# Optimization experiments

Measured on AMD Instinct MI355X. Metric: run time of the kernel, lower is better.

Reference implementation:

```python
import jax, jax.numpy as jnp
import numpy as np

N_NODES = 10000
N_EDGES = 80000
IN_DIM = 512
H1, H2, OUT_DIM = 4096, 1024, 7
NEG_SLOPE = 0.2


def _gat_layer(x, src, dst, W, a_src, a_dst, b, n_nodes):
    # x: [N, F_in] -> h: [N, F_out]
    h = x @ W
    # per-edge attention logits: a_src . h_i + a_dst . h_j (PyG GATConv, heads=1)
    e = jax.nn.leaky_relu((h @ a_src)[src] + (h @ a_dst)[dst], NEG_SLOPE)
    # segment softmax over destination nodes
    m = jax.ops.segment_max(e, dst, num_segments=n_nodes)
    ex = jnp.exp(e - m[dst])
    denom = jax.ops.segment_sum(ex, dst, num_segments=n_nodes)
    alpha = ex / denom[dst]
    # scatter-add weighted messages
    out = jax.ops.segment_sum(alpha[:, None] * h[src], dst, num_segments=n_nodes)
    return out + b


def setup_inputs() -> dict:
    key = jax.random.key(0)
    ks = jax.random.split(key, 16)
    s = 0.05
    inp = {
        "x": jax.random.normal(ks[0], (N_NODES, IN_DIM), dtype=jnp.float32),
        "edge_index": jax.random.randint(ks[1], (2, N_EDGES), 0, N_NODES, dtype=jnp.int32),
        "W1": jax.random.normal(ks[2], (IN_DIM, H1), dtype=jnp.float32) * s,
        "att_src1": jax.random.normal(ks[3], (H1,), dtype=jnp.float32) * s,
        "att_dst1": jax.random.normal(ks[4], (H1,), dtype=jnp.float32) * s,
        "b1": jnp.zeros((H1,), dtype=jnp.float32),
        "W2": jax.random.normal(ks[5], (H1, H2), dtype=jnp.float32) * s,
        "att_src2": jax.random.normal(ks[6], (H2,), dtype=jnp.float32) * s,
        "att_dst2": jax.random.normal(ks[7], (H2,), dtype=jnp.float32) * s,
        "b2": jnp.zeros((H2,), dtype=jnp.float32),
        "W3": jax.random.normal(ks[8], (H2, OUT_DIM), dtype=jnp.float32) * s,
        "att_src3": jax.random.normal(ks[9], (OUT_DIM,), dtype=jnp.float32) * s,
        "att_dst3": jax.random.normal(ks[10], (OUT_DIM,), dtype=jnp.float32) * s,
        "b3": jnp.zeros((OUT_DIM,), dtype=jnp.float32),
    }
    return inp


def reference(x, edge_index, W1, att_src1, att_dst1, b1,
              W2, att_src2, att_dst2, b2,
              W3, att_src3, att_dst3, b3):
    n = x.shape[0]
    loops = jnp.arange(n, dtype=edge_index.dtype)
    src = jnp.concatenate([edge_index[0], loops])  # add_self_loops=True
    dst = jnp.concatenate([edge_index[1], loops])
    h = _gat_layer(x, src, dst, W1, att_src1, att_dst1, b1, n)
    h = jax.nn.relu(h)  # dropout is identity in eval mode
    h = _gat_layer(h, src, dst, W2, att_src2, att_dst2, b2, n)
    h = jax.nn.relu(h)
    h = _gat_layer(h, src, dst, W3, att_src3, att_dst3, b3, n)
    return jax.nn.log_softmax(h, axis=1)
```

## Files before the change

kernel.cpp:

```cpp
#include <hip/hip_runtime.h>
#include <hip/hip_bf16.h>
#include <math.h>

#define NNODES  10000
#define NEDGES  80000
#define NTOT    90000
#define IN_DIM  512
#define H1_DIM  4096
#define H2_DIM  1024
#define ODIM    7
#define MAXDEG  128
#define NEG_SLOPE 0.2f

typedef __hip_bfloat16 bf16;
typedef __attribute__((ext_vector_type(8))) short short8;
typedef __attribute__((ext_vector_type(4))) float f32x4;

__device__ inline void unpack_bf2(unsigned u, float& lo, float& hi) {
    union { unsigned i; float f; } a, b;
    a.i = u << 16; b.i = u & 0xffff0000u;
    lo = a.f; hi = b.f;
}

#define ASYNC_COPY16(lds, g)                                                              \
    __builtin_amdgcn_global_load_lds((const __attribute__((address_space(1))) void*)(g),  \
                                     (__attribute__((address_space(3))) void*)(lds),      \
                                     16, 0, 0)

__global__ void build_bucket(const int* __restrict__ ei, int* cnt, int* bucket) {
    int k = blockIdx.x * blockDim.x + threadIdx.x;
    if (k >= NTOT) return;
    int s, d;
    if (k < NEDGES) { s = ei[k]; d = ei[NEDGES + k]; }
    else            { s = k - NEDGES; d = s; }
    int pos = atomicAdd(&cnt[d], 1);
    if (pos < MAXDEG) bucket[d * MAXDEG + pos] = s;
}

__global__ __launch_bounds__(256) void transpose_bf16(const float* __restrict__ W,
                                                      bf16* __restrict__ WT, int R, int C) {
    __shared__ float t[32][33];
    int c0 = blockIdx.x * 32, r0 = blockIdx.y * 32;
    int x = threadIdx.x & 31, y = threadIdx.x >> 5;
    #pragma unroll
    for (int dy = 0; dy < 32; dy += 8)
        t[y + dy][x] = W[(size_t)(r0 + y + dy) * C + c0 + x];
    __syncthreads();
    #pragma unroll
    for (int dy = 0; dy < 32; dy += 8)
        WT[(size_t)(c0 + y + dy) * R + r0 + x] = __float2bfloat16(t[x][y + dy]);
}

__global__ __launch_bounds__(256) void fold_att(const float* __restrict__ W,
                                                const float* __restrict__ a_s,
                                                const float* __restrict__ a_d,
                                                float* __restrict__ w_s,
                                                float* __restrict__ w_d, int C) {
    int r = blockIdx.x;
    const float* row = W + (size_t)r * C;
    float ss = 0.f, sd = 0.f;
    for (int j = threadIdx.x; j < C; j += 256) {
        float w = row[j];
        ss = fmaf(w, a_s[j], ss);
        sd = fmaf(w, a_d[j], sd);
    }
    #pragma unroll
    for (int off = 32; off > 0; off >>= 1) {
        ss += __shfl_down(ss, off);
        sd += __shfl_down(sd, off);
    }
    __shared__ float red[2][4];
    int wave = threadIdx.x >> 6;
    if ((threadIdx.x & 63) == 0) { red[0][wave] = ss; red[1][wave] = sd; }
    __syncthreads();
    if (threadIdx.x == 0) {
        w_s[r] = red[0][0] + red[0][1] + red[0][2] + red[0][3];
        w_d[r] = red[1][0] + red[1][1] + red[1][2] + red[1][3];
    }
}

__global__ __launch_bounds__(128) void dots_cvt1(const float* __restrict__ X,
                                                 const float* __restrict__ w_s,
                                                 const float* __restrict__ w_d,
                                                 float* __restrict__ s_src,
                                                 float* __restrict__ s_dst,
                                                 bf16* __restrict__ XB) {
    int n = blockIdx.x;
    int t = threadIdx.x;
    float4 xv = ((const float4*)(X + (size_t)n * IN_DIM))[t];
    float4 wsv = ((const float4*)w_s)[t];
    float4 wdv = ((const float4*)w_d)[t];
    bf16 o[4] = { __float2bfloat16(xv.x), __float2bfloat16(xv.y),
                  __float2bfloat16(xv.z), __float2bfloat16(xv.w) };
    *(uint2*)(XB + (size_t)n * IN_DIM + 4 * t) = *(uint2*)o;
    float ss = xv.x*wsv.x + xv.y*wsv.y + xv.z*wsv.z + xv.w*wsv.w;
    float sd = xv.x*wdv.x + xv.y*wdv.y + xv.z*wdv.z + xv.w*wdv.w;
    #pragma unroll
    for (int off = 32; off > 0; off >>= 1) {
        ss += __shfl_down(ss, off);
        sd += __shfl_down(sd, off);
    }
    __shared__ float red[2][2];
    int wave = t >> 6;
    if ((t & 63) == 0) { red[0][wave] = ss; red[1][wave] = sd; }
    __syncthreads();
    if (t == 0) {
        s_src[n] = red[0][0] + red[0][1];
        s_dst[n] = red[1][0] + red[1][1];
    }
}

__global__ __launch_bounds__(128) void agg1(const bf16* __restrict__ XB,
                                            const float* __restrict__ s_src,
                                            const float* __restrict__ s_dst,
                                            const int* __restrict__ bucket,
                                            const int* __restrict__ cnt,
                                            bf16* __restrict__ OUT) {
    int n = blockIdx.x;
    int c = min(cnt[n], MAXDEG);
    __shared__ float alpha[MAXDEG];
    __shared__ int   ssrc[MAXDEG];
    if (threadIdx.x < c) {
        int s = bucket[n * MAXDEG + threadIdx.x];
        ssrc[threadIdx.x] = s;
        float e = s_src[s] + s_dst[n];
        alpha[threadIdx.x] = (e > 0.f) ? e : NEG_SLOPE * e;
    }
    __syncthreads();
    if (threadIdx.x == 0) {
        float m = -1e30f;
        for (int j = 0; j < c; ++j) m = fmaxf(m, alpha[j]);
        float s = 0.f;
        for (int j = 0; j < c; ++j) { float ex = __expf(alpha[j] - m); alpha[j] = ex; s += ex; }
        float inv = 1.f / s;
        for (int j = 0; j < c; ++j) alpha[j] *= inv;
    }
    __syncthreads();
    int t = threadIdx.x;
    float acc[4] = {};
    for (int j = 0; j < c; ++j) {
        float a = alpha[j];
        uint2 raw = ((const uint2*)(XB + (size_t)ssrc[j] * IN_DIM))[t];
        float f0, f1, f2, f3;
        unpack_bf2(raw.x, f0, f1); unpack_bf2(raw.y, f2, f3);
        acc[0] = fmaf(a, f0, acc[0]); acc[1] = fmaf(a, f1, acc[1]);
        acc[2] = fmaf(a, f2, acc[2]); acc[3] = fmaf(a, f3, acc[3]);
    }
    bf16 o[4] = { __float2bfloat16(acc[0]), __float2bfloat16(acc[1]),
                  __float2bfloat16(acc[2]), __float2bfloat16(acc[3]) };
    *(uint2*)(OUT + (size_t)n * IN_DIM + 4 * t) = *(uint2*)o;
}

__global__ __launch_bounds__(128) void agg2_h3(const bf16* __restrict__ H,
                                               const float* __restrict__ s_src,
                                               const float* __restrict__ s_dst,
                                               const int* __restrict__ bucket,
                                               const int* __restrict__ cnt,
                                               const float* __restrict__ bias,
                                               const float* __restrict__ W3,
                                               const float* __restrict__ as3,
                                               const float* __restrict__ ad3,
                                               float* __restrict__ H3,
                                               float* __restrict__ s3_src,
                                               float* __restrict__ s3_dst) {
    int n = blockIdx.x;
    int c = min(cnt[n], MAXDEG);
    __shared__ float alpha[MAXDEG];
    __shared__ int   ssrc[MAXDEG];
    if (threadIdx.x < c) {
        int s = bucket[n * MAXDEG + threadIdx.x];
        ssrc[threadIdx.x] = s;
        float e = s_src[s] + s_dst[n];
        alpha[threadIdx.x] = (e > 0.f) ? e : NEG_SLOPE * e;
    }
    __syncthreads();
    if (threadIdx.x == 0) {
        float m = -1e30f;
        for (int j = 0; j < c; ++j) m = fmaxf(m, alpha[j]);
        float s = 0.f;
        for (int j = 0; j < c; ++j) { float ex = __expf(alpha[j] - m); alpha[j] = ex; s += ex; }
        float inv = 1.f / s;
        for (int j = 0; j < c; ++j) alpha[j] *= inv;
    }
    __syncthreads();
    int t = threadIdx.x;
    float acc[8] = {};
    for (int j = 0; j < c; ++j) {
        float a = alpha[j];
        uint4 raw = ((const uint4*)(H + (size_t)ssrc[j] * H2_DIM))[t];
        float f0, f1, f2, f3, f4, f5, f6, f7;
        unpack_bf2(raw.x, f0, f1); unpack_bf2(raw.y, f2, f3);
        unpack_bf2(raw.z, f4, f5); unpack_bf2(raw.w, f6, f7);
        acc[0] = fmaf(a, f0, acc[0]); acc[1] = fmaf(a, f1, acc[1]);
        acc[2] = fmaf(a, f2, acc[2]); acc[3] = fmaf(a, f3, acc[3]);
        acc[4] = fmaf(a, f4, acc[4]); acc[5] = fmaf(a, f5, acc[5]);
        acc[6] = fmaf(a, f6, acc[6]); acc[7] = fmaf(a, f7, acc[7]);
    }
    float p[ODIM] = {};
    #pragma unroll
    for (int k = 0; k < 8; ++k) {
        float v = fmaxf(acc[k] + bias[8 * t + k], 0.f);
        const float* wrow = W3 + (size_t)(8 * t + k) * ODIM;
        #pragma unroll
        for (int o = 0; o < ODIM; ++o)
            p[o] = fmaf(v, wrow[o], p[o]);
    }
    #pragma unroll
    for (int o = 0; o < ODIM; ++o)
        #pragma unroll
        for (int off = 32; off > 0; off >>= 1)
            p[o] += __shfl_down(p[o], off);
    __shared__ float red[2][ODIM];
    int wave = t >> 6;
    if ((t & 63) == 0)
        #pragma unroll
        for (int o = 0; o < ODIM; ++o) red[wave][o] = p[o];
    __syncthreads();
    if (t == 0) {
        float ss = 0.f, sd = 0.f;
        #pragma unroll
        for (int o = 0; o < ODIM; ++o) {
            float v = red[0][o] + red[1][o];
            H3[n * ODIM + o] = v;
            ss = fmaf(v, as3[o], ss);
            sd = fmaf(v, ad3[o], sd);
        }
        s3_src[n] = ss; s3_dst[n] = sd;
    }
}

template<int TM, int TN, bool BIASRELU, bool FUSEDOTS>
__global__ __launch_bounds__(256) void gemm_mfma(const bf16* __restrict__ A,
                                                 const bf16* __restrict__ BT,
                                                 const float* __restrict__ bias,
                                                 const float* __restrict__ w_s,
                                                 const float* __restrict__ w_d,
                                                 float* __restrict__ s_src,
                                                 float* __restrict__ s_dst,
                                                 bf16* __restrict__ C,
                                                 int M, int N, int K) {
    constexpr int NI = TM / 32;
    constexpr int NJ = TN / 32;
    __shared__ alignas(16) bf16 As[2][TM][32];
    __shared__ alignas(16) bf16 Bs[2][TN][32];
    const int tid  = threadIdx.x;
    const int wave = tid >> 6;
    const int lane = tid & 63;

    const int gx = gridDim.x;
    const int j  = blockIdx.y * gx + blockIdx.x;
    const int band = j / (8 * gx);
    const int kk2  = j - band * (8 * gx);
    const int by = (kk2 & 7) + 8 * band;
    const int bx = kk2 >> 3;
    const int row0 = by * TM;
    const int col0 = bx * TN;
    if (row0 >= M) return;

    const int wr0  = (wave >> 1) * (TM / 2);
    const int wc0  = (wave & 1) * (TN / 2);

    const int srow  = tid >> 2;
    const int skoff = ((tid & 3) ^ (srow & 3)) * 8;
    const bf16* agA0 = A + (size_t)min(row0 + srow, M - 1) * K + skoff;
    const bf16* agA1 = (TM == 128) ? A + (size_t)min(row0 + 64 + srow, M - 1) * K + skoff : nullptr;
    const bf16* bg0  = BT + (size_t)(col0 + srow) * K + skoff;
    const bf16* bg1  = (TN == 128) ? BT + (size_t)(col0 + 64 + srow) * K + skoff : nullptr;

    f32x4 acc[NI][NJ] = {};

    const int fRow  = lane & 15;
    const int fKoff = (((lane >> 4) ^ (fRow & 3))) * 8;

    for (int k0 = 0; k0 < K; k0 += 64) {
        #pragma unroll
        for (int h = 0; h < 2; ++h) {
            ASYNC_COPY16(&As[h][wave * 16][0], agA0 + h * 32);
            if constexpr (TM == 128)
                ASYNC_COPY16(&As[h][64 + wave * 16][0], agA1 + h * 32);
            ASYNC_COPY16(&Bs[h][wave * 16][0], bg0 + h * 32);
            if constexpr (TN == 128)
                ASYNC_COPY16(&Bs[h][64 + wave * 16][0], bg1 + h * 32);
        }
        agA0 += 64; bg0 += 64;
        if constexpr (TM == 128) agA1 += 64;
        if constexpr (TN == 128) bg1 += 64;
        __syncthreads();
        #pragma unroll
        for (int h = 0; h < 2; ++h) {
            short8 af[NI], bfr[NJ];
            #pragma unroll
            for (int i = 0; i < NI; ++i)
                af[i] = *(const short8*)&As[h][wr0 + i * 16 + fRow][fKoff];
            #pragma unroll
            for (int jj = 0; jj < NJ; ++jj)
                bfr[jj] = *(const short8*)&Bs[h][wc0 + jj * 16 + fRow][fKoff];
            #pragma unroll
            for (int i = 0; i < NI; ++i)
                #pragma unroll
                for (int jj = 0; jj < NJ; ++jj)
                    acc[i][jj] = __builtin_amdgcn_mfma_f32_16x16x32_bf16(af[i], bfr[jj], acc[i][jj], 0, 0, 0);
        }
        __syncthreads();
    }

    const int crow = (lane >> 4) * 4;
    const int ccol = lane & 15;
    #pragma unroll
    for (int i = 0; i < NI; ++i) {
        #pragma unroll
        for (int r = 0; r < 4; ++r) {
            int gm = row0 + wr0 + i * 16 + crow + r;
            float vss = 0.f, vsd = 0.f;
            if (gm < M) {
                #pragma unroll
                for (int jj = 0; jj < NJ; ++jj) {
                    int gn = col0 + wc0 + jj * 16 + ccol;
                    float v = acc[i][jj][r];
                    if (BIASRELU) v = fmaxf(v + bias[gn], 0.f);
                    C[(size_t)gm * N + gn] = __float2bfloat16(v);
                    if (FUSEDOTS) {
                        vss = fmaf(v, w_s[gn], vss);
                        vsd = fmaf(v, w_d[gn], vsd);
                    }
                }
            }
            if (FUSEDOTS) {
                #pragma unroll
                for (int m2 = 1; m2 < 16; m2 <<= 1) {
                    vss += __shfl_xor(vss, m2, 16);
                    vsd += __shfl_xor(vsd, m2, 16);
                }
                if ((lane & 15) == 0 && gm < M) {
                    atomicAdd(&s_src[gm], vss);
                    atomicAdd(&s_dst[gm], vsd);
                }
            }
        }
    }
}

__global__ __launch_bounds__(128) void aggregate3(const float* __restrict__ H3,
                                                  const float* __restrict__ s_src,
                                                  const float* __restrict__ s_dst,
                                                  const int* __restrict__ bucket,
                                                  const int* __restrict__ cnt,
                                                  const float* __restrict__ b3,
                                                  float* __restrict__ out) {
    int n = blockIdx.x;
    int c = min(cnt[n], MAXDEG);
    __shared__ float alpha[MAXDEG];
    __shared__ int   ssrc[MAXDEG];
    __shared__ float o[ODIM];
    if (threadIdx.x < c) {
        int s = bucket[n * MAXDEG + threadIdx.x];
        ssrc[threadIdx.x] = s;
        float e = s_src[s] + s_dst[n];
        alpha[threadIdx.x] = (e > 0.f) ? e : NEG_SLOPE * e;
    }
    __syncthreads();
    if (threadIdx.x == 0) {
        float m = -1e30f;
        for (int j = 0; j < c; ++j) m = fmaxf(m, alpha[j]);
        float s = 0.f;
        for (int j = 0; j < c; ++j) { float ex = __expf(alpha[j] - m); alpha[j] = ex; s += ex; }
        float inv = 1.f / s;
        for (int j = 0; j < c; ++j) alpha[j] *= inv;
    }
    __syncthreads();
    if (threadIdx.x < ODIM) {
        float acc = 0.f;
        for (int j = 0; j < c; ++j)
            acc = fmaf(alpha[j], H3[ssrc[j] * ODIM + threadIdx.x], acc);
        o[threadIdx.x] = acc + b3[threadIdx.x];
    }
    __syncthreads();
    if (threadIdx.x == 0) {
        float m = o[0];
        for (int k = 1; k < ODIM; ++k) m = fmaxf(m, o[k]);
        float s = 0.f;
        for (int k = 0; k < ODIM; ++k) s += __expf(o[k] - m);
        float lse = m + logf(s);
        for (int k = 0; k < ODIM; ++k) out[n * ODIM + k] = o[k] - lse;
    }
}

extern "C" void kernel_launch(void* const* d_in, const int* in_sizes, int n_in,
                              void* d_out, int out_size, void* d_ws, size_t ws_size,
                              hipStream_t stream) {
    const float* x   = (const float*)d_in[0];
    const int*   ei  = (const int*)  d_in[1];
    const float* W1  = (const float*)d_in[2];
    const float* as1 = (const float*)d_in[3];
    const float* ad1 = (const float*)d_in[4];
    const float* b1  = (const float*)d_in[5];
    const float* W2  = (const float*)d_in[6];
    const float* as2 = (const float*)d_in[7];
    const float* ad2 = (const float*)d_in[8];
    const float* b2  = (const float*)d_in[9];
    const float* W3  = (const float*)d_in[10];
    const float* as3 = (const float*)d_in[11];
    const float* ad3 = (const float*)d_in[12];
    const float* b3  = (const float*)d_in[13];
    float* outp = (float*)d_out;

    char* p = (char*)d_ws;
    bf16*  x2     = (bf16*)p;   p += (size_t)NNODES * H1_DIM * sizeof(bf16);
    bf16*  r2     = (bf16*)p;   p += (size_t)NNODES * H2_DIM * sizeof(bf16);
    bf16*  r3     = (bf16*)p;   p += (size_t)NNODES * H2_DIM * sizeof(bf16);
    bf16*  W2T    = (bf16*)p;   p += (size_t)H2_DIM * H1_DIM * sizeof(bf16);
    float* h3     = (float*)p;  p += (size_t)NNODES * ODIM * sizeof(float);
    float* ssrc   = (float*)p;  p += NNODES * sizeof(float);
    float* sdst   = (float*)p;  p += NNODES * sizeof(float);
    float* ssrc3  = (float*)p;  p += NNODES * sizeof(float);
    float* sdst3  = (float*)p;  p += NNODES * sizeof(float);
    float* w1s    = (float*)p;  p += IN_DIM * sizeof(float);
    float* w1d    = (float*)p;  p += IN_DIM * sizeof(float);
    float* w2s    = (float*)p;  p += H1_DIM * sizeof(float);
    float* w2d    = (float*)p;  p += H1_DIM * sizeof(float);
    int*   cnt    = (int*)p;    p += NNODES * sizeof(int);
    int*   bucket = (int*)p;    p += (size_t)NNODES * MAXDEG * sizeof(int);
    size_t required = (size_t)(p - (char*)d_ws);
    if (ws_size < required) return;

    bf16* xb    = x2;
    bf16* aggxb = r2;
    bf16* h2    = r2;
    bf16* W1T   = r3;

    hipMemsetAsync(cnt, 0, NNODES * sizeof(int), stream);
    build_bucket<<<(NTOT + 255) / 256, 256, 0, stream>>>(ei, cnt, bucket);

    fold_att<<<IN_DIM, 256, 0, stream>>>(W1, as1, ad1, w1s, w1d, H1_DIM);
    dots_cvt1<<<NNODES, 128, 0, stream>>>(x, w1s, w1d, ssrc, sdst, xb);
    agg1<<<NNODES, 128, 0, stream>>>(xb, ssrc, sdst, bucket, cnt, aggxb);

    const int nRow = (NNODES + 127) / 128;
    const int nRowPad = ((nRow + 7) / 8) * 8;

    fold_att<<<H1_DIM, 256, 0, stream>>>(W2, as2, ad2, w2s, w2d, H2_DIM);
    hipMemsetAsync(ssrc, 0, 2 * NNODES * sizeof(float), stream);
    {
        dim3 tg(H1_DIM / 32, IN_DIM / 32);
        transpose_bf16<<<tg, 256, 0, stream>>>(W1, W1T, IN_DIM, H1_DIM);
        dim3 g(H1_DIM / 128, nRowPad);
        gemm_mfma<128, 128, true, true><<<g, 256, 0, stream>>>(aggxb, W1T, b1, w2s, w2d,
                                                               ssrc, sdst, x2, NNODES, H1_DIM, IN_DIM);
    }

    {
        dim3 tg(H2_DIM / 32, H1_DIM / 32);
        transpose_bf16<<<tg, 256, 0, stream>>>(W2, W2T, H1_DIM, H2_DIM);
        dim3 g(H2_DIM / 64, nRowPad);
        gemm_mfma<128, 64, false, false><<<g, 256, 0, stream>>>(x2, W2T, nullptr, nullptr, nullptr,
                                                                nullptr, nullptr, h2, NNODES, H2_DIM, H1_DIM);
    }

    agg2_h3<<<NNODES, 128, 0, stream>>>(h2, ssrc, sdst, bucket, cnt, b2,
                                        W3, as3, ad3, h3, ssrc3, sdst3);

    aggregate3<<<NNODES, 128, 0, stream>>>(h3, ssrc3, sdst3, bucket, cnt, b3, outp);
}
```

Baseline: 432.5 us.

## Fuse attention folding into weight transpose and double-buffer GEMM k-loop

Measured after the change: 440.1 us. About the same (+1.8%).

```diff
diff --git a/kernel.cpp b/kernel.cpp
--- a/kernel.cpp
+++ b/kernel.cpp
@@ -37,46 +37,36 @@
     if (pos < MAXDEG) bucket[d * MAXDEG + pos] = s;
 }
 
-__global__ __launch_bounds__(256) void transpose_bf16(const float* __restrict__ W,
-                                                      bf16* __restrict__ WT, int R, int C) {
+__global__ __launch_bounds__(256) void transpose_fold(const float* __restrict__ W,
+                                                      bf16* __restrict__ WT,
+                                                      const float* __restrict__ a_s,
+                                                      const float* __restrict__ a_d,
+                                                      float* __restrict__ w_s,
+                                                      float* __restrict__ w_d,
+                                                      int R, int C) {
     __shared__ float t[32][33];
     int c0 = blockIdx.x * 32, r0 = blockIdx.y * 32;
     int x = threadIdx.x & 31, y = threadIdx.x >> 5;
-    #pragma unroll
-    for (int dy = 0; dy < 32; dy += 8)
-        t[y + dy][x] = W[(size_t)(r0 + y + dy) * C + c0 + x];
+    float asv = a_s[c0 + x], adv = a_d[c0 + x];
+    #pragma unroll
+    for (int dy = 0; dy < 32; dy += 8) {
+        float w = W[(size_t)(r0 + y + dy) * C + c0 + x];
+        t[y + dy][x] = w;
+        float ps = w * asv, pd = w * adv;
+        #pragma unroll
+        for (int off = 16; off > 0; off >>= 1) {
+            ps += __shfl_down(ps, off, 32);
+            pd += __shfl_down(pd, off, 32);
+        }
+        if (x == 0) {
+            atomicAdd(&w_s[r0 + y + dy], ps);
+            atomicAdd(&w_d[r0 + y + dy], pd);
+        }
+    }
     __syncthreads();
     #pragma unroll
     for (int dy = 0; dy < 32; dy += 8)
         WT[(size_t)(c0 + y + dy) * R + r0 + x] = __float2bfloat16(t[x][y + dy]);
-}
-
-__global__ __launch_bounds__(256) void fold_att(const float* __restrict__ W,
-                                                const float* __restrict__ a_s,
-                                                const float* __restrict__ a_d,
-                                                float* __restrict__ w_s,
-                                                float* __restrict__ w_d, int C) {
-    int r = blockIdx.x;
-    const float* row = W + (size_t)r * C;
-    float ss = 0.f, sd = 0.f;
-    for (int j = threadIdx.x; j < C; j += 256) {
-        float w = row[j];
-        ss = fmaf(w, a_s[j], ss);
-        sd = fmaf(w, a_d[j], sd);
-    }
-    #pragma unroll
-    for (int off = 32; off > 0; off >>= 1) {
-        ss += __shfl_down(ss, off);
-        sd += __shfl_down(sd, off);
-    }
-    __shared__ float red[2][4];
-    int wave = threadIdx.x >> 6;
-    if ((threadIdx.x & 63) == 0) { red[0][wave] = ss; red[1][wave] = sd; }
-    __syncthreads();
-    if (threadIdx.x == 0) {
-        w_s[r] = red[0][0] + red[0][1] + red[0][2] + red[0][3];
-        w_d[r] = red[1][0] + red[1][1] + red[1][2] + red[1][3];
-    }
 }
 
 __global__ __launch_bounds__(128) void dots_cvt1(const float* __restrict__ X,
@@ -250,57 +240,55 @@
     const int gx = gridDim.x;
     const int j  = blockIdx.y * gx + blockIdx.x;
     const int band = j / (8 * gx);
-    const int kk2  = j - band * (8 * gx);
-    const int by = (kk2 & 7) + 8 * band;
-    const int bx = kk2 >> 3;
+    const int r8   = j - band * (8 * gx);
+    const int by = (r8 & 7) + 8 * band;
+    const int bx = r8 >> 3;
     const int row0 = by * TM;
     const int col0 = bx * TN;
     if (row0 >= M) return;
 
-    const int wr0  = (wave >> 1) * (TM / 2);
-    const int wc0  = (wave & 1) * (TN / 2);
+    const int wr0 = (wave >> 1) * (TM / 2);
+    const int wc0 = (wave & 1) * (TN / 2);
 
     const int srow  = tid >> 2;
     const int skoff = ((tid & 3) ^ (srow & 3)) * 8;
-    const bf16* agA0 = A + (size_t)min(row0 + srow, M - 1) * K + skoff;
-    const bf16* agA1 = (TM == 128) ? A + (size_t)min(row0 + 64 + srow, M - 1) * K + skoff : nullptr;
-    const bf16* bg0  = BT + (size_t)(col0 + srow) * K + skoff;
-    const bf16* bg1  = (TN == 128) ? BT + (size_t)(col0 + 64 + srow) * K + skoff : nullptr;
+    const bf16* a0 = A + (size_t)min(row0 + srow, M - 1) * K + skoff;
+    const bf16* a1 = A + (size_t)min(row0 + 64 + srow, M - 1) * K + skoff;
+    const bf16* b0 = BT + (size_t)(col0 + srow) * K + skoff;
+    const bf16* b1 = BT + (size_t)(col0 + 64 + srow) * K + skoff;
 
     f32x4 acc[NI][NJ] = {};
-
     const int fRow  = lane & 15;
-    const int fKoff = (((lane >> 4) ^ (fRow & 3))) * 8;
-
-    for (int k0 = 0; k0 < K; k0 += 64) {
-        #pragma unroll
-        for (int h = 0; h < 2; ++h) {
-            ASYNC_COPY16(&As[h][wave * 16][0], agA0 + h * 32);
-            if constexpr (TM == 128)
-                ASYNC_COPY16(&As[h][64 + wave * 16][0], agA1 + h * 32);
-            ASYNC_COPY16(&Bs[h][wave * 16][0], bg0 + h * 32);
-            if constexpr (TN == 128)
-                ASYNC_COPY16(&Bs[h][64 + wave * 16][0], bg1 + h * 32);
+    const int fKoff = ((lane >> 4) ^ (fRow & 3)) * 8;
+
+    const int NIT = K >> 5;
+    ASYNC_COPY16(&As[0][wave * 16][0],      a0);
+    ASYNC_COPY16(&As[0][64 + wave * 16][0], a1);
+    ASYNC_COPY16(&Bs[0][wave * 16][0],      b0);
+    ASYNC_COPY16(&Bs[0][64 + wave * 16][0], b1);
+    __syncthreads();
+
+    for (int it = 0; it < NIT; ++it) {
+        const int cb = it & 1, nb = cb ^ 1;
+        if (it + 1 < NIT) {
+            const int ko = (it + 1) << 5;
+            ASYNC_COPY16(&As[nb][wave * 16][0],      a0 + ko);
+            ASYNC_COPY16(&As[nb][64 + wave * 16][0], a1 + ko);
+            ASYNC_COPY16(&Bs[nb][wave * 16][0],      b0 + ko);
+            ASYNC_COPY16(&Bs[nb][64 + wave * 16][0], b1 + ko);
         }
-        agA0 += 64; bg0 += 64;
-        if constexpr (TM == 128) agA1 += 64;
-        if constexpr (TN == 128) bg1 += 64;
-        __syncthreads();
-        #pragma unroll
-        for (int h = 0; h < 2; ++h) {
-            short8 af[NI], bfr[NJ];
-            #pragma unroll
-            for (int i = 0; i < NI; ++i)
-                af[i] = *(const short8*)&As[h][wr0 + i * 16 + fRow][fKoff];
+        short8 af[NI], bfr[NJ];
+        #pragma unroll
+        for (int i = 0; i < NI; ++i)
+            af[i] = *(const short8*)&As[cb][wr0 + i * 16 + fRow][fKoff];
+        #pragma unroll
+        for (int jj = 0; jj < NJ; ++jj)
+            bfr[jj] = *(const short8*)&Bs[cb][wc0 + jj * 16 + fRow][fKoff];
+        #pragma unroll
+        for (int i = 0; i < NI; ++i)
             #pragma unroll
             for (int jj = 0; jj < NJ; ++jj)
-                bfr[jj] = *(const short8*)&Bs[h][wc0 + jj * 16 + fRow][fKoff];
-            #pragma unroll
-            for (int i = 0; i < NI; ++i)
-                #pragma unroll
-                for (int jj = 0; jj < NJ; ++jj)
-                    acc[i][jj] = __builtin_amdgcn_mfma_f32_16x16x32_bf16(af[i], bfr[jj], acc[i][jj], 0, 0, 0);
-        }
+                acc[i][jj] = __builtin_amdgcn_mfma_f32_16x16x32_bf16(af[i], bfr[jj], acc[i][jj], 0, 0, 0);
         __syncthreads();
     }
 
@@ -429,31 +417,32 @@
     bf16* W1T   = r3;
 
     hipMemsetAsync(cnt, 0, NNODES * sizeof(int), stream);
+    hipMemsetAsync(w1s, 0, (2 * IN_DIM + 2 * H1_DIM) * sizeof(float), stream);
     build_bucket<<<(NTOT + 255) / 256, 256, 0, stream>>>(ei, cnt, bucket);
 
-    fold_att<<<IN_DIM, 256, 0, stream>>>(W1, as1, ad1, w1s, w1d, H1_DIM);
+    {
+        dim3 tg1(H1_DIM / 32, IN_DIM / 32);
+        transpose_fold<<<tg1, 256, 0, stream>>>(W1, W1T, as1, ad1, w1s, w1d, IN_DIM, H1_DIM);
+        dim3 tg2(H2_DIM / 32, H1_DIM / 32);
+        transpose_fold<<<tg2, 256, 0, stream>>>(W2, W2T, as2, ad2, w2s, w2d, H1_DIM, H2_DIM);
+    }
+
     dots_cvt1<<<NNODES, 128, 0, stream>>>(x, w1s, w1d, ssrc, sdst, xb);
     agg1<<<NNODES, 128, 0, stream>>>(xb, ssrc, sdst, bucket, cnt, aggxb);
 
-    const int nRow = (NNODES + 127) / 128;
-    const int nRowPad = ((nRow + 7) / 8) * 8;
-
-    fold_att<<<H1_DIM, 256, 0, stream>>>(W2, as2, ad2, w2s, w2d, H2_DIM);
+    const int nRowPad = ((((NNODES + 127) / 128) + 7) / 8) * 8;
+
     hipMemsetAsync(ssrc, 0, 2 * NNODES * sizeof(float), stream);
     {
-        dim3 tg(H1_DIM / 32, IN_DIM / 32);
-        transpose_bf16<<<tg, 256, 0, stream>>>(W1, W1T, IN_DIM, H1_DIM);
         dim3 g(H1_DIM / 128, nRowPad);
         gemm_mfma<128, 128, true, true><<<g, 256, 0, stream>>>(aggxb, W1T, b1, w2s, w2d,
                                                                ssrc, sdst, x2, NNODES, H1_DIM, IN_DIM);
     }
 
     {
-        dim3 tg(H2_DIM / 32, H1_DIM / 32);
-        transpose_bf16<<<tg, 256, 0, stream>>>(W2, W2T, H1_DIM, H2_DIM);
-        dim3 g(H2_DIM / 64, nRowPad);
-        gemm_mfma<128, 64, false, false><<<g, 256, 0, stream>>>(x2, W2T, nullptr, nullptr, nullptr,
-                                                                nullptr, nullptr, h2, NNODES, H2_DIM, H1_DIM);
+        dim3 g(H2_DIM / 128, nRowPad);
+        gemm_mfma<128, 128, false, false><<<g, 256, 0, stream>>>(x2, W2T, nullptr, nullptr, nullptr,
+                                                                 nullptr, nullptr, h2, NNODES, H2_DIM, H1_DIM);
     }
 
     agg2_h3<<<NNODES, 128, 0, stream>>>(h2, ssrc, sdst, bucket, cnt, b2,
```
